# Kernel tuning notes

Measured on AMD Instinct MI355X. Metric: run time of the kernel, lower is better.

## Reference

```python
import jax, jax.numpy as jnp
import numpy as np

EPS = 1e-6
GROUPS = 32
SCALE = 1.0 / np.float32(512.0) ** 0.5


def setup_inputs() -> dict:
    key = jax.random.key(0)
    ks = jax.random.split(key, 8)
    b, c, h, w = 4, 512, 64, 64
    std = 0.02
    return {
        "x": jax.random.normal(ks[0], (b, c, h, w), dtype=jnp.float32),
        "gamma": jnp.ones((c,), jnp.float32),
        "beta": jnp.zeros((c,), jnp.float32),
        "wq_w": jax.random.normal(ks[1], (c, c), jnp.float32) * std,
        "wq_b": jax.random.normal(ks[2], (c,), jnp.float32) * std,
        "wk_w": jax.random.normal(ks[3], (c, c), jnp.float32) * std,
        "wk_b": jax.random.normal(ks[4], (c,), jnp.float32) * std,
        "wv_w": jax.random.normal(ks[5], (c, c), jnp.float32) * std,
        "wv_b": jax.random.normal(ks[6], (c,), jnp.float32) * std,
        "out_w": jax.random.normal(ks[7], (c, c), jnp.float32) * std,
        "out_b": jnp.zeros((c,), jnp.float32),
    }


def reference(x, gamma, beta, wq_w, wq_b, wk_w, wk_b, wv_w, wv_b, out_w, out_b):
    b, c, h, w = x.shape
    # GroupNorm(32 groups, eps=1e-6, affine)
    xg = x.reshape(b, GROUPS, c // GROUPS, h, w)
    mean = xg.mean(axis=(2, 3, 4), keepdims=True)
    var = ((xg - mean) ** 2).mean(axis=(2, 3, 4), keepdims=True)
    xn = ((xg - mean) * jax.lax.rsqrt(var + EPS)).reshape(b, c, h, w)
    xn = xn * gamma[None, :, None, None] + beta[None, :, None, None]
    # flatten spatial -> tokens: [b, N, c]
    t = xn.reshape(b, c, h * w).transpose(0, 2, 1)
    q = t @ wq_w.T + wq_b
    k = t @ wk_w.T + wk_b
    v = t @ wv_w.T + wv_b
    scores = jnp.einsum('bnc,bmc->bnm', q, k) * SCALE  # [b, N, N]
    attn = jax.nn.softmax(scores, axis=2)
    o = jnp.einsum('bnm,bmc->bnc', attn, v)
    o = o @ out_w.T + out_b
    return o.transpose(0, 2, 1).reshape(b, c, h, w) + x
```

## Files before the change

kernel.cpp:

```cpp
#include <hip/hip_runtime.h>
#include <hip/hip_fp8.h>

typedef unsigned short u16;
typedef unsigned char u8;
typedef unsigned int u32;
typedef short bf16x8 __attribute__((ext_vector_type(8)));
typedef float f32x4 __attribute__((ext_vector_type(4)));
typedef u16 u16x4 __attribute__((ext_vector_type(4)));

#define SCALE_Q 0.044194173824159216f

__device__ __forceinline__ u16 f2b(float f){
  unsigned u = __float_as_uint(f);
  u += 0x7fffu + ((u >> 16) & 1u);
  return (u16)(u >> 16);
}

__device__ __forceinline__ u8 f2e4(float f){
  return __hip_fp8_e4m3(f).__x;
}

__device__ __forceinline__ void gload16(const void* g, void* l){
  __builtin_amdgcn_global_load_lds(
      (const __attribute__((address_space(1))) void*)g,
      (__attribute__((address_space(3))) void*)l, 16, 0, 0);
}

__device__ __forceinline__ float qsum16(float v){
  v += __shfl_xor(v, 1); v += __shfl_xor(v, 2);
  v += __shfl_xor(v, 4); v += __shfl_xor(v, 8);
  return v;
}

__global__ __launch_bounds__(256) void gn_stats(const float* __restrict__ x,
                                                float* __restrict__ stats){
  int bg = blockIdx.x;
  const float4* p4 = (const float4*)(x + (size_t)bg * 65536);
  float s = 0.f, ss = 0.f;
  for (int i = threadIdx.x; i < 16384; i += 256){
    float4 v = p4[i];
    s  += v.x + v.y + v.z + v.w;
    ss += v.x*v.x + v.y*v.y + v.z*v.z + v.w*v.w;
  }
  for (int off = 32; off; off >>= 1){
    s  += __shfl_down(s, off);
    ss += __shfl_down(ss, off);
  }
  __shared__ float as_[4], bs_[4];
  int wid = threadIdx.x >> 6, lid = threadIdx.x & 63;
  if (lid == 0){ as_[wid] = s; bs_[wid] = ss; }
  __syncthreads();
  if (threadIdx.x == 0){
    float S = as_[0]+as_[1]+as_[2]+as_[3], SS = bs_[0]+bs_[1]+bs_[2]+bs_[3];
    float mean = S * (1.f/65536.f);
    float var  = SS * (1.f/65536.f) - mean*mean;
    stats[2*bg]   = mean;
    stats[2*bg+1] = rsqrtf(var + 1e-6f);
  }
}

__global__ __launch_bounds__(256) void gn_apply_T(const float* __restrict__ x,
                                                  const float* __restrict__ stats,
                                                  const float* __restrict__ gamma,
                                                  const float* __restrict__ beta,
                                                  u16* __restrict__ t){
  __shared__ float tile[32][33];
  int nb = blockIdx.x, cb = blockIdx.y, b = blockIdx.z;
  int tx = threadIdx.x & 31, ty = threadIdx.x >> 5;
  int n0 = nb * 32, c0 = cb * 32;
  #pragma unroll
  for (int i = 0; i < 4; i++){
    int ch = c0 + ty + i*8;
    float mean = stats[2*((b<<5) + (ch>>4))];
    float rstd = stats[2*((b<<5) + (ch>>4)) + 1];
    float v = x[(((size_t)b*512 + ch) << 12) + n0 + tx];
    tile[ty + i*8][tx] = (v - mean) * rstd * gamma[ch] + beta[ch];
  }
  __syncthreads();
  #pragma unroll
  for (int i = 0; i < 4; i++){
    int n = n0 + ty + i*8;
    int ch = c0 + tx;
    t[((size_t)((b<<12) + n))*512 + ch] = f2b(tile[tx][ty + i*8]);
  }
}

__global__ __launch_bounds__(256) void w2bf(const float* __restrict__ a,
                                            const float* __restrict__ b,
                                            const float* __restrict__ c,
                                            const float* __restrict__ d,
                                            u16* __restrict__ o){
  int idx = blockIdx.x * 256 + threadIdx.x;
  int which = idx >> 16;
  const float4* src = (const float4*)(which == 0 ? a : which == 1 ? b : which == 2 ? c : d);
  float4 v = src[idx & 65535];
  u16x4 pk;
  pk.x = f2b(v.x); pk.y = f2b(v.y); pk.z = f2b(v.z); pk.w = f2b(v.w);
  *(u16x4*)(o + (size_t)idx*4) = pk;
}

__global__ __launch_bounds__(256, 2) void qkv_gemm(const u16* __restrict__ A,
                                                   const u16* __restrict__ Wcat,
                                                   const float* __restrict__ qbias,
                                                   const float* __restrict__ kbias,
                                                   const float* __restrict__ vbias,
                                                   u8* __restrict__ qo,
                                                   u8* __restrict__ ko,
                                                   u8* __restrict__ vo){
  __shared__ __align__(16) u16 SMEM[8192];
  u16* As = SMEM;
  u16* Bs = SMEM + 4096;
  const int t = threadIdx.x;
  const int w = t >> 6, ln = t & 63;
  const int wr = w >> 1, wc = w & 1;
  const int q4 = ln >> 4, l15 = ln & 15;
  const int y = blockIdx.y;
  const int mat = y >> 2, yb = y & 3;
  const int row0 = blockIdx.x * 128;
  const u16* Ab = A    + (size_t)row0 * 512;
  const u16* Bb = Wcat + (size_t)y * 128 * 512;
  f32x4 acc[4][4];
  #pragma unroll
  for (int i = 0; i < 4; i++)
    #pragma unroll
    for (int j = 0; j < 4; j++){
      acc[i][j][0]=0.f; acc[i][j][1]=0.f; acc[i][j][2]=0.f; acc[i][j][3]=0.f;
    }
  for (int kt = 0; kt < 16; ++kt){
    #pragma unroll
    for (int i = 0; i < 2; i++){
      int idx = i*256 + t;
      gload16(Ab + (size_t)(idx>>2)*512 + kt*32 + (idx&3)*8, As + (size_t)idx*8);
      gload16(Bb + (size_t)(idx>>2)*512 + kt*32 + (idx&3)*8, Bs + (size_t)idx*8);
    }
    __syncthreads();
    bf16x8 af[4], bf[4];
    #pragma unroll
    for (int mt = 0; mt < 4; mt++)
      af[mt] = *(const bf16x8*)(As + (wr*64 + mt*16 + l15)*32 + q4*8);
    #pragma unroll
    for (int nt = 0; nt < 4; nt++)
      bf[nt] = *(const bf16x8*)(Bs + (wc*64 + nt*16 + l15)*32 + q4*8);
    #pragma unroll
    for (int mt = 0; mt < 4; mt++)
      #pragma unroll
      for (int nt = 0; nt < 4; nt++)
        acc[mt][nt] = __builtin_amdgcn_mfma_f32_16x16x32_bf16(af[mt], bf[nt], acc[mt][nt], 0, 0, 0);
    __syncthreads();
  }
  const int bb = row0 >> 12;
  const int tile0 = (row0 >> 6) & 63;
  const int col0 = yb*128 + wc*64;
  u8* Ls = (u8*)SMEM;

  if (mat == 0){
    #pragma unroll
    for (int nt = 0; nt < 4; nt++){
      int n = col0 + nt*16 + l15;
      float bv = qbias[n];
      #pragma unroll
      for (int mt = 0; mt < 4; mt++){
        int m0 = row0 + wr*64 + mt*16 + q4*4;
        #pragma unroll
        for (int r = 0; r < 4; r++)
          qo[(size_t)(m0 + r)*512 + n] = f2e4(acc[mt][nt][r] + bv);
      }
    }
  } else if (mat == 1){
    #pragma unroll
    for (int nt = 0; nt < 4; nt++){
      int n = col0 + nt*16 + l15;
      float bv = kbias[n];
      int ksl = wc*2 + (nt >> 1);
      int c3  = ((nt & 1)*2 + (l15 >> 3));
      #pragma unroll
      for (int mt = 0; mt < 4; mt++){
        #pragma unroll
        for (int r = 0; r < 4; r++){
          int kr = mt*16 + q4*4 + r;
          int chunk = c3 ^ ((kr >> 2) & 3);
          Ls[(wr*4 + ksl)*2048 + kr*32 + chunk*8 + (l15 & 7)] = f2e4(acc[mt][nt][r] + bv);
        }
      }
    }
    __syncthreads();
    #pragma unroll
    for (int i = 0; i < 4; i++){
      int ci = i*256 + t;
      int ri = ci >> 7, t2 = ri >> 2, ksl2 = ri & 3;
      u8* dst = ko + ((size_t)(bb*64 + tile0 + t2))*32768
                   + (size_t)(yb*4 + ksl2)*2048 + (size_t)(ci & 127)*16;
      *(float4*)dst = *(const float4*)(Ls + (size_t)ci*16);
    }
  } else {
    #pragma unroll
    for (int nt = 0; nt < 4; nt++){
      int n = col0 + nt*16 + l15;
      float bv = vbias[n];
      int nl = n & 127;
      #pragma unroll
      for (int mt = 0; mt < 4; mt++){
        int kv = mt*16 + q4*4;
        u32 pk = (u32)f2e4(acc[mt][nt][0] + bv)
               | ((u32)f2e4(acc[mt][nt][1] + bv) << 8)
               | ((u32)f2e4(acc[mt][nt][2] + bv) << 16)
               | ((u32)f2e4(acc[mt][nt][3] + bv) << 24);
        int phys = (kv >> 3) ^ (n & 7);
        *(u32*)(Ls + wr*8192 + nl*64 + phys*8 + (kv & 4)) = pk;
      }
    }
    __syncthreads();
    #pragma unroll
    for (int i = 0; i < 4; i++){
      int ci = i*256 + t;
      int t2 = ci >> 9;
      u8* dst = vo + ((size_t)(bb*64 + tile0 + t2))*32768
                   + (size_t)yb*8192 + (size_t)(ci & 511)*16;
      *(float4*)dst = *(const float4*)(Ls + (size_t)ci*16);
    }
  }
}

__global__ __launch_bounds__(256, 2) void out_gemm(const u16* __restrict__ A,
                                                   const u16* __restrict__ Bw,
                                                   const float* __restrict__ bias,
                                                   float* __restrict__ out,
                                                   const float* __restrict__ resid){
  __shared__ __align__(16) u16 As[128*32];
  __shared__ __align__(16) u16 Bs[128*32];
  const int t = threadIdx.x;
  const int w = t >> 6, ln = t & 63;
  const int wr = w >> 1, wc = w & 1;
  const int q4 = ln >> 4, l15 = ln & 15;
  const u16* Ab = A  + (size_t)blockIdx.x * 128 * 512;
  const u16* Bb = Bw + (size_t)blockIdx.y * 128 * 512;
  f32x4 acc[4][4];
  #pragma unroll
  for (int i = 0; i < 4; i++)
    #pragma unroll
    for (int j = 0; j < 4; j++){
      acc[i][j][0]=0.f; acc[i][j][1]=0.f; acc[i][j][2]=0.f; acc[i][j][3]=0.f;
    }
  for (int kt = 0; kt < 16; ++kt){
    #pragma unroll
    for (int i = 0; i < 2; i++){
      int idx = i*256 + t;
      gload16(Ab + (size_t)(idx>>2)*512 + kt*32 + (idx&3)*8, As + (size_t)idx*8);
      gload16(Bb + (size_t)(idx>>2)*512 + kt*32 + (idx&3)*8, Bs + (size_t)idx*8);
    }
    __syncthreads();
    bf16x8 af[4], bf[4];
    #pragma unroll
    for (int mt = 0; mt < 4; mt++)
      af[mt] = *(const bf16x8*)(As + (wr*64 + mt*16 + l15)*32 + q4*8);
    #pragma unroll
    for (int nt = 0; nt < 4; nt++)
      bf[nt] = *(const bf16x8*)(Bs + (wc*64 + nt*16 + l15)*32 + q4*8);
    #pragma unroll
    for (int mt = 0; mt < 4; mt++)
      #pragma unroll
      for (int nt = 0; nt < 4; nt++)
        acc[mt][nt] = __builtin_amdgcn_mfma_f32_16x16x32_bf16(af[mt], bf[nt], acc[mt][nt], 0, 0, 0);
    __syncthreads();
  }
  const int row0 = blockIdx.x*128 + wr*64;
  const int col0 = blockIdx.y*128 + wc*64;
  #pragma unroll
  for (int nt = 0; nt < 4; nt++){
    int n = col0 + nt*16 + l15;
    float bv = bias[n];
    #pragma unroll
    for (int mt = 0; mt < 4; mt++){
      int m0 = row0 + mt*16 + q4*4;
      int bb = m0 >> 12, tok = m0 & 4095;
      size_t base = (((size_t)(bb*512 + n)) << 12) + tok;
      float4 xr = *(const float4*)(resid + base);
      float4 ov;
      ov.x = acc[mt][nt][0] + bv + xr.x;
      ov.y = acc[mt][nt][1] + bv + xr.y;
      ov.z = acc[mt][nt][2] + bv + xr.z;
      ov.w = acc[mt][nt][3] + bv + xr.w;
      *(float4*)(out + base) = ov;
    }
  }
}

__global__ __launch_bounds__(512, 4) void attn_fwd(const u8* __restrict__ q,
                                                   const u8* __restrict__ kt,
                                                   const u8* __restrict__ vt,
                                                   u16* __restrict__ outO){
  __shared__ __align__(16) u8 Kb[2][32768];
  __shared__ __align__(16) u8 Pb[2][32*72];
  __shared__ __align__(16) float lL[128];

  const int t = threadIdx.x, w = t >> 6, ln = t & 63;
  const int q4 = ln >> 4, l15 = ln & 15;
  const int rt = w >> 2, kvq = w & 3;
  const int b = blockIdx.y, q0 = blockIdx.x * 32;
  const u8* kbase = kt + ((size_t)b << 21);
  const u8* vbase = vt + ((size_t)b << 21);

  long qf[16];
  {
    const u8* qr = q + (size_t)((b<<12) + q0 + rt*16 + l15) * 512;
    #pragma unroll
    for (int ks = 0; ks < 16; ks++) qf[ks] = *(const long*)(qr + ks*32 + q4*8);
  }
  f32x4 oacc[2][4];
  #pragma unroll
  for (int i = 0; i < 2; i++)
    #pragma unroll
    for (int j = 0; j < 4; j++){
      oacc[i][j][0]=0.f; oacc[i][j][1]=0.f; oacc[i][j][2]=0.f; oacc[i][j][3]=0.f;
    }
  f32x4 lrow; lrow[0]=0.f; lrow[1]=0.f; lrow[2]=0.f; lrow[3]=0.f;

  const int kr = kvq*16 + l15;
  const int ko = kr*32 + ((q4 ^ ((kr >> 2) & 3)) << 3);

  #pragma unroll
  for (int i = 0; i < 4; i++){
    int ci = i*512 + t;
    gload16(kbase + (size_t)ci*16, &Kb[0][ci*16]);
  }
  __syncthreads();

  #pragma unroll 1
  for (int j = 0; j < 64; ++j){
    if (j < 63){
      const u8* kn = kbase + ((size_t)(j + 1) << 15);
      u8* kd = Kb[(j + 1) & 1];
      #pragma unroll
      for (int i = 0; i < 4; i++){
        int ci = i*512 + t;
        gload16(kn + (size_t)ci*16, kd + ci*16);
      }
    }
    long vf0[4], vf1[4];
    if (j > 0){
      const u8* vtile = vbase + ((size_t)(j - 1) << 15);
      #pragma unroll
      for (int ct = 0; ct < 4; ct++){
        int ch = 64*w + ct*16 + l15;
        int swz = ch & 7;
        const u8* vr = vtile + (size_t)ch*64;
        vf0[ct] = *(const long*)(vr + ((q4 ^ swz) << 3));
        vf1[ct] = *(const long*)(vr + (((4 + q4) ^ swz) << 3));
      }
    }
    const u8* Kp = Kb[j & 1];
    f32x4 sA0, sA1;
    sA0[0]=0.f;sA0[1]=0.f;sA0[2]=0.f;sA0[3]=0.f;
    sA1[0]=0.f;sA1[1]=0.f;sA1[2]=0.f;sA1[3]=0.f;
    __builtin_amdgcn_s_setprio(1);
    #pragma unroll
    for (int k2 = 0; k2 < 8; k2++){
      const u8* e0 = Kp + (2*k2)*2048;
      const u8* e1 = Kp + (2*k2 + 1)*2048;
      long ka0 = *(const long*)(e0 + ko);
      long ka1 = *(const long*)(e1 + ko);
      sA0 = __builtin_amdgcn_mfma_f32_16x16x32_fp8_fp8(qf[2*k2],   ka0, sA0, 0, 0, 0);
      sA1 = __builtin_amdgcn_mfma_f32_16x16x32_fp8_fp8(qf[2*k2+1], ka1, sA1, 0, 0, 0);
    }
    if (j > 0){
      const u8* Pp = Pb[(j - 1) & 1];
      long pf00 = *(const long*)(Pp + l15*72 + q4*8);
      long pf01 = *(const long*)(Pp + l15*72 + 32 + q4*8);
      long pf10 = *(const long*)(Pp + (16 + l15)*72 + q4*8);
      long pf11 = *(const long*)(Pp + (16 + l15)*72 + 32 + q4*8);
      #pragma unroll
      for (int ct = 0; ct < 4; ct++){
        f32x4 a0 = oacc[0][ct], a1 = oacc[1][ct];
        a0 = __builtin_amdgcn_mfma_f32_16x16x32_fp8_fp8(pf00, vf0[ct], a0, 0, 0, 0);
        a1 = __builtin_amdgcn_mfma_f32_16x16x32_fp8_fp8(pf10, vf0[ct], a1, 0, 0, 0);
        a0 = __builtin_amdgcn_mfma_f32_16x16x32_fp8_fp8(pf01, vf1[ct], a0, 0, 0, 0);
        a1 = __builtin_amdgcn_mfma_f32_16x16x32_fp8_fp8(pf11, vf1[ct], a1, 0, 0, 0);
        oacc[0][ct] = a0; oacc[1][ct] = a1;
      }
    }
    __builtin_amdgcn_s_setprio(0);
    #pragma unroll
    for (int r = 0; r < 4; r++){
      float e0 = __expf((sA0[r] + sA1[r]) * SCALE_Q);
      lrow[r] += e0;
      int row = rt*16 + q4*4 + r;
      Pb[j & 1][row*72 + kvq*16 + l15] = f2e4(e0);
    }
    __syncthreads();
  }

  {
    const u8* vtile = vbase + ((size_t)63 << 15);
    long vf0[4], vf1[4];
    #pragma unroll
    for (int ct = 0; ct < 4; ct++){
      int ch = 64*w + ct*16 + l15;
      int swz = ch & 7;
      const u8* vr = vtile + (size_t)ch*64;
      vf0[ct] = *(const long*)(vr + ((q4 ^ swz) << 3));
      vf1[ct] = *(const long*)(vr + (((4 + q4) ^ swz) << 3));
    }
    const u8* Pp = Pb[1];
    long pf00 = *(const long*)(Pp + l15*72 + q4*8);
    long pf01 = *(const long*)(Pp + l15*72 + 32 + q4*8);
    long pf10 = *(const long*)(Pp + (16 + l15)*72 + q4*8);
    long pf11 = *(const long*)(Pp + (16 + l15)*72 + 32 + q4*8);
    #pragma unroll
    for (int ct = 0; ct < 4; ct++){
      f32x4 a0 = oacc[0][ct], a1 = oacc[1][ct];
      a0 = __builtin_amdgcn_mfma_f32_16x16x32_fp8_fp8(pf00, vf0[ct], a0, 0, 0, 0);
      a1 = __builtin_amdgcn_mfma_f32_16x16x32_fp8_fp8(pf10, vf0[ct], a1, 0, 0, 0);
      a0 = __builtin_amdgcn_mfma_f32_16x16x32_fp8_fp8(pf01, vf1[ct], a0, 0, 0, 0);
      a1 = __builtin_amdgcn_mfma_f32_16x16x32_fp8_fp8(pf11, vf1[ct], a1, 0, 0, 0);
      oacc[0][ct] = a0; oacc[1][ct] = a1;
    }
  }

  {
    f32x4 ls;
    #pragma unroll
    for (int r = 0; r < 4; r++) ls[r] = qsum16(lrow[r]);
    if (l15 == 0) *(f32x4*)&lL[kvq*32 + rt*16 + q4*4] = ls;
  }
  __syncthreads();
  #pragma unroll
  for (int rr = 0; rr < 2; rr++){
    #pragma unroll
    for (int r = 0; r < 4; r++){
      int row = rr*16 + q4*4 + r;
      float inv = 1.f / (lL[row] + lL[32 + row] + lL[64 + row] + lL[96 + row]);
      u16* op = outO + ((size_t)b << 21) + (size_t)(q0 + row)*512 + 64*w + l15;
      #pragma unroll
      for (int ct = 0; ct < 4; ct++)
        op[ct*16] = f2b(oacc[rr][ct][r] * inv);
    }
  }
}

extern "C" void kernel_launch(void* const* d_in, const int* in_sizes, int n_in,
                              void* d_out, int out_size, void* d_ws, size_t ws_size,
                              hipStream_t stream){
  const float* x     = (const float*)d_in[0];
  const float* gamma = (const float*)d_in[1];
  const float* beta  = (const float*)d_in[2];
  const float* wq_w  = (const float*)d_in[3];
  const float* wq_b  = (const float*)d_in[4];
  const float* wk_w  = (const float*)d_in[5];
  const float* wk_b  = (const float*)d_in[6];
  const float* wv_w  = (const float*)d_in[7];
  const float* wv_b  = (const float*)d_in[8];
  const float* out_w = (const float*)d_in[9];
  const float* out_b = (const float*)d_in[10];

  char* ws = (char*)d_ws;
  float* stats = (float*)ws;
  u16* tbuf = (u16*)(ws + 4096);
  size_t off = 4096 + (size_t)16*1024*1024;
  u16* Wcat = (u16*)(ws + off); off += (size_t)4*512*512*2;
  u8*  qb   = (u8*)(ws + off);  off += (size_t)16*1024*1024;
  u8*  ktb  = (u8*)(ws + off);  off += (size_t)16*1024*1024;
  u8*  vtb  = (u8*)(ws + off);  off += (size_t)16*1024*1024;

  gn_stats<<<128, 256, 0, stream>>>(x, stats);
  gn_apply_T<<<dim3(128, 16, 4), 256, 0, stream>>>(x, stats, gamma, beta, tbuf);
  w2bf<<<1024, 256, 0, stream>>>(wq_w, wk_w, wv_w, out_w, Wcat);
  u16* Wo = Wcat + 3*512*512;
  qkv_gemm<<<dim3(128, 12), 256, 0, stream>>>(tbuf, Wcat, wq_b, wk_b, wv_b,
                                              qb, ktb, vtb);
  attn_fwd<<<dim3(128, 4), 512, 0, stream>>>(qb, ktb, vtb, tbuf);
  out_gemm<<<dim3(128, 4), 256, 0, stream>>>(tbuf, Wo, out_b, (float*)d_out, x);
}
```

Baseline: 327.4 us.

## Use 16x16x128 scaled fp8 MFMA for QK^T and pack P stores

Replaces the sixteen 16x16x32 fp8 MFMAs that compute QK^T scores with four 16x16x128 f8f6f4 scaled MFMAs. Operands are swapped so the score tile is transposed, which lets each lane produce four consecutive key columns for one query row. Those four exps are packed into a single 32-bit fp8 store to LDS. The row-sum reduction shrinks to a cross-quad shuffle, and the P-fragment LDS reads are hoisted above the QK loop. The goal is fewer MFMA issues and LDS stores per tile, at the cost of wider register operands and reliance on the unit scale encoding being correct.

```diff
diff --git a/kernel.cpp b/kernel.cpp
--- a/kernel.cpp
+++ b/kernel.cpp
@@ -7,6 +7,8 @@
 typedef short bf16x8 __attribute__((ext_vector_type(8)));
 typedef float f32x4 __attribute__((ext_vector_type(4)));
 typedef u16 u16x4 __attribute__((ext_vector_type(4)));
+typedef int i32x8 __attribute__((ext_vector_type(8)));
+typedef long l64x4 __attribute__((ext_vector_type(4)));
 
 #define SCALE_Q 0.044194173824159216f
 
@@ -24,12 +26,6 @@
   __builtin_amdgcn_global_load_lds(
       (const __attribute__((address_space(1))) void*)g,
       (__attribute__((address_space(3))) void*)l, 16, 0, 0);
-}
-
-__device__ __forceinline__ float qsum16(float v){
-  v += __shfl_xor(v, 1); v += __shfl_xor(v, 2);
-  v += __shfl_xor(v, 4); v += __shfl_xor(v, 8);
-  return v;
 }
 
 __global__ __launch_bounds__(256) void gn_stats(const float* __restrict__ x,
@@ -300,11 +296,12 @@
   const u8* kbase = kt + ((size_t)b << 21);
   const u8* vbase = vt + ((size_t)b << 21);
 
-  long qf[16];
+  i32x8 qm[4];
   {
     const u8* qr = q + (size_t)((b<<12) + q0 + rt*16 + l15) * 512;
     #pragma unroll
-    for (int ks = 0; ks < 16; ks++) qf[ks] = *(const long*)(qr + ks*32 + q4*8);
+    for (int kk = 0; kk < 4; kk++)
+      qm[kk] = *(const i32x8*)(qr + kk*128 + q4*32);
   }
   f32x4 oacc[2][4];
   #pragma unroll
@@ -313,10 +310,14 @@
     for (int j = 0; j < 4; j++){
       oacc[i][j][0]=0.f; oacc[i][j][1]=0.f; oacc[i][j][2]=0.f; oacc[i][j][3]=0.f;
     }
-  f32x4 lrow; lrow[0]=0.f; lrow[1]=0.f; lrow[2]=0.f; lrow[3]=0.f;
+  float lrow = 0.f;
 
   const int kr = kvq*16 + l15;
-  const int ko = kr*32 + ((q4 ^ ((kr >> 2) & 3)) << 3);
+  const int sw = (kr >> 2) & 3;
+  const int kof0 = q4*2048 + kr*32 + (((0 ^ sw)) << 3);
+  const int kof1 = q4*2048 + kr*32 + (((1 ^ sw)) << 3);
+  const int kof2 = q4*2048 + kr*32 + (((2 ^ sw)) << 3);
+  const int kof3 = q4*2048 + kr*32 + (((3 ^ sw)) << 3);
 
   #pragma unroll
   for (int i = 0; i < 4; i++){
@@ -337,6 +338,7 @@
       }
     }
     long vf0[4], vf1[4];
+    long pf00, pf01, pf10, pf11;
     if (j > 0){
       const u8* vtile = vbase + ((size_t)(j - 1) << 15);
       #pragma unroll
@@ -347,6 +349,11 @@
         vf0[ct] = *(const long*)(vr + ((q4 ^ swz) << 3));
         vf1[ct] = *(const long*)(vr + (((4 + q4) ^ swz) << 3));
       }
+      const u8* Pp = Pb[(j - 1) & 1];
+      pf00 = *(const long*)(Pp + l15*72 + q4*8);
+      pf01 = *(const long*)(Pp + l15*72 + 32 + q4*8);
+      pf10 = *(const long*)(Pp + (16 + l15)*72 + q4*8);
+      pf11 = *(const long*)(Pp + (16 + l15)*72 + 32 + q4*8);
     }
     const u8* Kp = Kb[j & 1];
     f32x4 sA0, sA1;
@@ -354,20 +361,22 @@
     sA1[0]=0.f;sA1[1]=0.f;sA1[2]=0.f;sA1[3]=0.f;
     __builtin_amdgcn_s_setprio(1);
     #pragma unroll
-    for (int k2 = 0; k2 < 8; k2++){
-      const u8* e0 = Kp + (2*k2)*2048;
-      const u8* e1 = Kp + (2*k2 + 1)*2048;
-      long ka0 = *(const long*)(e0 + ko);
-      long ka1 = *(const long*)(e1 + ko);
-      sA0 = __builtin_amdgcn_mfma_f32_16x16x32_fp8_fp8(qf[2*k2],   ka0, sA0, 0, 0, 0);
-      sA1 = __builtin_amdgcn_mfma_f32_16x16x32_fp8_fp8(qf[2*k2+1], ka1, sA1, 0, 0, 0);
+    for (int kk = 0; kk < 4; kk++){
+      const u8* e = Kp + kk*8192;
+      l64x4 kl;
+      kl[0] = *(const long*)(e + kof0);
+      kl[1] = *(const long*)(e + kof1);
+      kl[2] = *(const long*)(e + kof2);
+      kl[3] = *(const long*)(e + kof3);
+      i32x8 kb = __builtin_bit_cast(i32x8, kl);
+      if (kk & 1)
+        sA1 = __builtin_amdgcn_mfma_scale_f32_16x16x128_f8f6f4(
+                  kb, qm[kk], sA1, 0, 0, 0, 0x7F, 0, 0x7F);
+      else
+        sA0 = __builtin_amdgcn_mfma_scale_f32_16x16x128_f8f6f4(
+                  kb, qm[kk], sA0, 0, 0, 0, 0x7F, 0, 0x7F);
     }
     if (j > 0){
-      const u8* Pp = Pb[(j - 1) & 1];
-      long pf00 = *(const long*)(Pp + l15*72 + q4*8);
-      long pf01 = *(const long*)(Pp + l15*72 + 32 + q4*8);
-      long pf10 = *(const long*)(Pp + (16 + l15)*72 + q4*8);
-      long pf11 = *(const long*)(Pp + (16 + l15)*72 + 32 + q4*8);
       #pragma unroll
       for (int ct = 0; ct < 4; ct++){
         f32x4 a0 = oacc[0][ct], a1 = oacc[1][ct];
@@ -379,12 +388,20 @@
       }
     }
     __builtin_amdgcn_s_setprio(0);
-    #pragma unroll
-    for (int r = 0; r < 4; r++){
-      float e0 = __expf((sA0[r] + sA1[r]) * SCALE_Q);
-      lrow[r] += e0;
-      int row = rt*16 + q4*4 + r;
-      Pb[j & 1][row*72 + kvq*16 + l15] = f2e4(e0);
+    {
+      float e0 = __expf((sA0[0] + sA1[0]) * SCALE_Q);
+      float e1 = __expf((sA0[1] + sA1[1]) * SCALE_Q);
+      float e2 = __expf((sA0[2] + sA1[2]) * SCALE_Q);
+      float e3 = __expf((sA0[3] + sA1[3]) * SCALE_Q);
+      lrow += (e0 + e1) + (e2 + e3);
+#if defined(__has_builtin) && __has_builtin(__builtin_amdgcn_cvt_pk_fp8_f32)
+      int pk = __builtin_amdgcn_cvt_pk_fp8_f32(e0, e1, 0, false);
+      pk = __builtin_amdgcn_cvt_pk_fp8_f32(e2, e3, pk, true);
+#else
+      u32 pk = (u32)f2e4(e0) | ((u32)f2e4(e1) << 8)
+             | ((u32)f2e4(e2) << 16) | ((u32)f2e4(e3) << 24);
+#endif
+      *(u32*)(Pb[j & 1] + (rt*16 + l15)*72 + kvq*16 + q4*4) = pk;
     }
     __syncthreads();
   }
@@ -417,10 +434,10 @@
   }
 
   {
-    f32x4 ls;
-    #pragma unroll
-    for (int r = 0; r < 4; r++) ls[r] = qsum16(lrow[r]);
-    if (l15 == 0) *(f32x4*)&lL[kvq*32 + rt*16 + q4*4] = ls;
+    float v = lrow;
+    v += __shfl_xor(v, 16);
+    v += __shfl_xor(v, 32);
+    if (ln < 16) lL[kvq*32 + rt*16 + l15] = v;
   }
   __syncthreads();
   #pragma unroll
```

New measurement: 519.8 us. 1.59x slower.
